# Performance work log

Hardware: AMD Instinct MI355X
Metric: run time of the kernel (lower is better)

Reference implementation:

```python
import jax, jax.numpy as jnp
import numpy as np

D_MODEL, D_K, D_V, H, M = 1024, 64, 64, 16, 40


def setup_inputs() -> dict:
    key = jax.random.key(0)
    ks = jax.random.split(key, 16)
    b, nq, nk = 8, 1024, 1024
    inp = {
        "queries": jax.random.normal(ks[0], (b, nq, D_MODEL), jnp.float32),
        "keys": jax.random.normal(ks[1], (b, nk, D_MODEL), jnp.float32),
        "values": jax.random.normal(ks[2], (b, nk, D_MODEL), jnp.float32),
        "attention_mask": jax.random.randint(ks[3], (b, H, nq, nk), 0, 2) > 0,
        # Linear params, parametrized as x @ W + b (W has shape (in, out)).
        "Wq": jax.random.normal(ks[4], (D_MODEL, H * D_K), jnp.float32) * 0.03,
        "bq": jnp.zeros((H * D_K,), jnp.float32),
        "Wk": jax.random.normal(ks[5], (D_MODEL, H * D_K), jnp.float32) * 0.03,
        "bk": jnp.zeros((H * D_K,), jnp.float32),
        "Wv": jax.random.normal(ks[6], (D_MODEL, H * D_V), jnp.float32) * 0.03,
        "bv": jnp.zeros((H * D_V,), jnp.float32),
        "Wo": jax.random.normal(ks[7], (H * D_V, D_MODEL), jnp.float32) * 0.03,
        "bo": jnp.zeros((D_MODEL,), jnp.float32),
        # Memory slots: m_k ~ N(0, 1/d_k), m_v ~ N(0, 1/m), shape (1, m, h*d)
        "m_k": jax.random.normal(ks[8], (1, M, H * D_K), jnp.float32) / D_K,
        "m_v": jax.random.normal(ks[9], (1, M, H * D_V), jnp.float32) / M,
    }
    return inp


def reference(queries, keys, values, attention_mask, Wq, bq, Wk, bk, Wv, bv, Wo, bo, m_k, m_v):
    b, nq, _ = queries.shape
    nk = keys.shape[1]
    scale = jnp.asarray(np.sqrt(D_K), jnp.float32)

    # scaled memory slots, broadcast over batch
    mk = scale * jnp.broadcast_to(m_k, (b, M, H * D_K))
    mv = jnp.asarray(np.sqrt(M), jnp.float32) * jnp.broadcast_to(m_v, (b, M, H * D_V))

    q = (queries @ Wq + bq).reshape(b, nq, H, D_K).transpose(0, 2, 1, 3)       # b h nq dk
    k = jnp.concatenate([keys @ Wk + bk, mk], axis=1)                           # b (nk+m) h*dk
    k = k.reshape(b, nk + M, H, D_K).transpose(0, 2, 1, 3)                      # b h (nk+m) dk
    v = jnp.concatenate([values @ Wv + bv, mv], axis=1)
    v = v.reshape(b, nk + M, H, D_V).transpose(0, 2, 1, 3)                      # b h (nk+m) dv

    att = jnp.einsum('bhqd,bhkd->bhqk', q, k) / scale                           # b h nq (nk+m)
    # mask only real keys; memory slots always attendable
    att_real = jnp.where(attention_mask, -jnp.inf, att[:, :, :, :nk])
    att = jnp.concatenate([att_real, att[:, :, :, nk:]], axis=-1)
    att = jax.nn.softmax(att, axis=-1)

    out = jnp.einsum('bhqk,bhkd->bhqd', att, v)
    out = out.transpose(0, 2, 1, 3).reshape(b, nq, H * D_V)
    out = out @ Wo + bo
    return out, att
```

## Files before the change

### kernel.cpp

```cpp
#include <hip/hip_runtime.h>
#include <hip/hip_bf16.h>


#define B_ 8
#define NQ 1024
#define NK 1024
#define DM 1024
#define H_ 16
#define DK 64
#define NKM 1064
#define NKP 1104
#define PSTR 280

typedef __attribute__((ext_vector_type(8))) short bf16x8;
typedef __attribute__((ext_vector_type(4))) float f32x4;
typedef __attribute__((ext_vector_type(4))) short short4v;

static __device__ __forceinline__ short f2bf(float x) {
    __hip_bfloat16 h = __float2bfloat16(x);
    return __builtin_bit_cast(short, h);
}
static __device__ __forceinline__ float bf2f(short s) {
    unsigned int u = ((unsigned int)(unsigned short)s) << 16;
    return __builtin_bit_cast(float, u);
}

static __device__ __forceinline__ bf16x8 pack8(const float* __restrict__ p) {
    float4 f0 = *(const float4*)p;
    float4 f1 = *(const float4*)(p + 4);
    bf16x8 a;
    a[0] = f2bf(f0.x); a[1] = f2bf(f0.y); a[2] = f2bf(f0.z); a[3] = f2bf(f0.w);
    a[4] = f2bf(f1.x); a[5] = f2bf(f1.y); a[6] = f2bf(f1.z); a[7] = f2bf(f1.w);
    return a;
}

static __device__ __forceinline__ void gload16(const short* g, short* l) {
    __builtin_amdgcn_global_load_lds(
        (__attribute__((address_space(1))) void*)const_cast<short*>(g),
        (__attribute__((address_space(3))) void*)l, 16, 0, 0);
}

__global__ void detect_mask_kernel(const unsigned int* __restrict__ m, int n_dwords,
                                   int* __restrict__ flag) {
    __shared__ int any_big;
    if (threadIdx.x == 0) any_big = 0;
    __syncthreads();
    for (int i = threadIdx.x; i < n_dwords; i += blockDim.x)
        if (m[i] > 1u) any_big = 1;
    __syncthreads();
    if (threadIdx.x == 0) *flag = any_big ? 0 : 1;
}

__global__ void transpose_w_kernel(const float* __restrict__ W, short* __restrict__ WT) {
    __shared__ float t[32][33];
    int tx = threadIdx.x & 31, ty = threadIdx.x >> 5;
    int k0 = blockIdx.x * 32, n0 = blockIdx.y * 32;
#pragma unroll
    for (int r = 0; r < 4; r++)
        t[ty + 8 * r][tx] = W[(size_t)(k0 + ty + 8 * r) * DM + n0 + tx];
    __syncthreads();
#pragma unroll
    for (int r = 0; r < 4; r++)
        WT[(size_t)(n0 + ty + 8 * r) * DM + k0 + tx] = f2bf(t[tx][ty + 8 * r]);
}

__global__ void convert_bf16_kernel(const float* __restrict__ a, const float* __restrict__ b,
                                    const float* __restrict__ c, short* __restrict__ out) {
    const size_t NT = (size_t)B_ * NQ * DM;
    const size_t total = NT * 3;
    size_t i = ((size_t)blockIdx.x * 256 + threadIdx.x) * 8;
    const size_t step = (size_t)gridDim.x * 256 * 8;
    for (; i < total; i += step) {
        const float* src = (i < NT) ? (a + i) : (i < 2 * NT) ? (b + (i - NT)) : (c + (i - 2 * NT));
        *(bf16x8*)(out + i) = pack8(src);
    }
}

__global__ void fill_mem_kernel(const float* __restrict__ m_k, const float* __restrict__ m_v,
                                short* __restrict__ Kh, short* __restrict__ Vt) {
    int blk = blockIdx.x;
    int bh = blk / 20, rb = blk % 20;
    int r = rb * 4 + (threadIdx.x >> 6);
    int d = threadIdx.x & 63;
    int h = bh & 15;
    float kv = 0.f, vv = 0.f;
    if (r < 40) {
        kv = 8.0f * m_k[(size_t)(r * H_ + h) * DK + d];
        vv = 6.324555320336759f * m_v[(size_t)(r * H_ + h) * DK + d];
    }
    int kk = 1024 + r;
    Kh[((size_t)bh * NKP + kk) * 64 + d] = f2bf(kv);
    Vt[((size_t)bh * 64 + d) * NKP + kk] = f2bf(vv);
}

template <int MODE>
__global__ __launch_bounds__(256) void gemm_tile_kernel(
    const short* __restrict__ Ab, const short* __restrict__ BT,
    const float* __restrict__ bias,
    float* __restrict__ outF, short* __restrict__ outB) {
    __shared__ short As[2][4096];
    __shared__ short Bs[2][4096];

    const int tid = threadIdx.x;
    const int lane = tid & 63;
    const int wid = tid >> 6;
    int swz = (blockIdx.x & 7) * 64 + (blockIdx.x >> 3);
    const int mt = swz >> 3, nt = swz & 7;
    const int brow = mt * 128, bcol = nt * 128;
    const int wr = wid >> 1, wc = wid & 1;
    const int l15 = lane & 15, lg = lane >> 4;

    f32x4 acc[4][4];
#pragma unroll
    for (int m = 0; m < 4; m++)
#pragma unroll
        for (int n = 0; n < 4; n++) acc[m][n] = f32x4{0.f, 0.f, 0.f, 0.f};

    auto stage = [&](int buf, int k0) {
#pragma unroll
        for (int i = 0; i < 2; i++) {
            int c = tid + i * 256;
            int row = c >> 2, slot = c & 3;
            int base = (c & ~63) * 8;
            gload16(Ab + (size_t)(brow + row) * DM + k0 + slot * 8, &As[buf][base]);
            gload16(BT + (size_t)(bcol + row) * DM + k0 + slot * 8, &Bs[buf][base]);
        }
    };

    stage(0, 0);
    for (int kt = 0; kt < 32; ++kt) {
        __syncthreads();
        if (kt + 1 < 32) stage((kt + 1) & 1, (kt + 1) * 32);
        const short* Ab_ = As[kt & 1];
        const short* Bb_ = Bs[kt & 1];
        bf16x8 a[4], b[4];
#pragma unroll
        for (int m = 0; m < 4; m++)
            a[m] = *(const bf16x8*)(Ab_ + (wr * 64 + m * 16 + l15) * 32 + lg * 8);
#pragma unroll
        for (int n = 0; n < 4; n++)
            b[n] = *(const bf16x8*)(Bb_ + (wc * 64 + n * 16 + l15) * 32 + lg * 8);
#pragma unroll
        for (int m = 0; m < 4; m++)
#pragma unroll
            for (int n = 0; n < 4; n++)
                acc[m][n] = __builtin_amdgcn_mfma_f32_16x16x32_bf16(a[m], b[n], acc[m][n], 0, 0, 0);
    }

#pragma unroll
    for (int n = 0; n < 4; n++) {
        int col = bcol + wc * 64 + n * 16 + l15;
        float bval = bias[col];
#pragma unroll
        for (int m = 0; m < 4; m++) {
            int row0 = brow + wr * 64 + m * 16 + lg * 4;
            if (MODE == 3) {
#pragma unroll
                for (int r = 0; r < 4; r++)
                    outF[(size_t)(row0 + r) * DM + col] = acc[m][n][r] + bval;
            } else if (MODE == 0) {
                int h = col >> 6, d = col & 63;
#pragma unroll
                for (int r = 0; r < 4; r++) {
                    int row = row0 + r;
                    int b = row >> 10, q = row & 1023;
                    outB[((size_t)(b * H_ + h) * NQ + q) * 64 + d] = f2bf(acc[m][n][r] + bval);
                }
            } else if (MODE == 1) {
                int h = col >> 6, d = col & 63;
#pragma unroll
                for (int r = 0; r < 4; r++) {
                    int row = row0 + r;
                    int b = row >> 10, kk = row & 1023;
                    outB[((size_t)(b * H_ + h) * NKP + kk) * 64 + d] = f2bf(acc[m][n][r] + bval);
                }
            } else {
                int h = col >> 6, d = col & 63;
                int b = row0 >> 10, kk0 = row0 & 1023;
                short4v sv;
#pragma unroll
                for (int r = 0; r < 4; r++) sv[r] = f2bf(acc[m][n][r] + bval);
                *(short4v*)(outB + ((size_t)(b * H_ + h) * 64 + d) * NKP + kk0) = sv;
            }
        }
    }
}

__global__ __launch_bounds__(256, 4) void attn_fused_kernel(
    const short* __restrict__ Qh, const short* __restrict__ Kh,
    const short* __restrict__ Vt,
    const unsigned char* __restrict__ mb, const int* __restrict__ mi,
    const int* __restrict__ flag,
    float* __restrict__ att, short* __restrict__ Ow) {
    __shared__ short Pl[4][16][PSTR];
    __shared__ float redS[4][16];

    int swz = (blockIdx.x & 7) * 1024 + (blockIdx.x >> 3);
    int bh = swz >> 6;
    int q0 = (swz & 63) * 16;
    int wid = threadIdx.x >> 6;
    int lane = threadIdx.x & 63;
    int l15 = lane & 15, lg = lane >> 4;

    const short* Qb = Qh + (size_t)bh * NQ * 64;
    const short* Kb = Kh + (size_t)bh * NKP * 64;
    const short* Vb = Vt + (size_t)bh * 64 * NKP;
    const int is32 = *flag;

    bf16x8 aq0 = *(const bf16x8*)(Qb + (size_t)(q0 + l15) * 64 + lg * 8);
    bf16x8 aq1 = *(const bf16x8*)(Qb + (size_t)(q0 + l15) * 64 + 32 + lg * 8);

    size_t qrow = (size_t)bh * NQ + q0 + l15;
    const int kkw = wid * 272;
    const int rofs = ((l15 >> 2) << 3) + (l15 & 3);

    f32x4 po[4];
#pragma unroll
    for (int dt = 0; dt < 4; dt++) po[dt] = f32x4{0.f, 0.f, 0.f, 0.f};
    float rs = 0.f;

#pragma unroll 2
    for (int pp = 0; pp < 9; ++pp) {
        int ofs = pp * 32 + lg * 8;
        int base = kkw + pp * 32;
        int kkb = base + lg * 8;
        const short* Kr0 = Kb + (size_t)(base + rofs) * 64;
        bf16x8 k0a = *(const bf16x8*)(Kr0 + lg * 8);
        bf16x8 k0b = *(const bf16x8*)(Kr0 + 32 + lg * 8);
        bf16x8 k1a = *(const bf16x8*)(Kr0 + 256 + lg * 8);
        bf16x8 k1b = *(const bf16x8*)(Kr0 + 256 + 32 + lg * 8);
        bf16x8 bv0 = *(const bf16x8*)(Vb + (size_t)(l15) * NKP + kkb);
        bf16x8 bv1 = *(const bf16x8*)(Vb + (size_t)(16 + l15) * NKP + kkb);
        bf16x8 bv2 = *(const bf16x8*)(Vb + (size_t)(32 + l15) * NKP + kkb);
        bf16x8 bv3 = *(const bf16x8*)(Vb + (size_t)(48 + l15) * NKP + kkb);
        unsigned mlo = 0, mhi = 0;
        if (kkb < NK) {
            if (is32) {
                int4 ma = *(const int4*)(mi + qrow * NK + kkb);
                int4 mc = *(const int4*)(mi + qrow * NK + kkb + 4);
                mlo = (ma.x ? 1u : 0u) | (ma.y ? 0x100u : 0u) |
                      (ma.z ? 0x10000u : 0u) | (ma.w ? 0x1000000u : 0u);
                mhi = (mc.x ? 1u : 0u) | (mc.y ? 0x100u : 0u) |
                      (mc.z ? 0x10000u : 0u) | (mc.w ? 0x1000000u : 0u);
            } else {
                uint2 mu = *(const uint2*)(mb + qrow * NK + kkb);
                mlo = mu.x; mhi = mu.y;
            }
        }
        f32x4 s0 = {0.f, 0.f, 0.f, 0.f}, s1 = {0.f, 0.f, 0.f, 0.f};
        s0 = __builtin_amdgcn_mfma_f32_16x16x32_bf16(k0a, aq0, s0, 0, 0, 0);
        s0 = __builtin_amdgcn_mfma_f32_16x16x32_bf16(k0b, aq1, s0, 0, 0, 0);
        s1 = __builtin_amdgcn_mfma_f32_16x16x32_bf16(k1a, aq0, s1, 0, 0, 0);
        s1 = __builtin_amdgcn_mfma_f32_16x16x32_bf16(k1b, aq1, s1, 0, 0, 0);
        bool live = (kkb < NKM) && (ofs < 272);
        bf16x8 pa;
        float e;
#pragma unroll
        for (int r = 0; r < 4; r++) {
            e = (live && (((mlo >> (8 * r)) & 0xffu) == 0u)) ? __expf(s0[r] * 0.125f) : 0.f;
            rs += e;
            pa[r] = f2bf(e);
        }
#pragma unroll
        for (int r = 0; r < 4; r++) {
            e = (live && (((mhi >> (8 * r)) & 0xffu) == 0u)) ? __expf(s1[r] * 0.125f) : 0.f;
            rs += e;
            pa[4 + r] = f2bf(e);
        }
        po[0] = __builtin_amdgcn_mfma_f32_16x16x32_bf16(pa, bv0, po[0], 0, 0, 0);
        po[1] = __builtin_amdgcn_mfma_f32_16x16x32_bf16(pa, bv1, po[1], 0, 0, 0);
        po[2] = __builtin_amdgcn_mfma_f32_16x16x32_bf16(pa, bv2, po[2], 0, 0, 0);
        po[3] = __builtin_amdgcn_mfma_f32_16x16x32_bf16(pa, bv3, po[3], 0, 0, 0);
        if (ofs < 272)
            *(bf16x8*)(&Pl[wid][l15][ofs]) = pa;
    }

    rs += __shfl_xor(rs, 16);
    rs += __shfl_xor(rs, 32);
    if (lg == 0) redS[wid][l15] = rs;
    __syncthreads();
    float invq = 1.f / (redS[0][l15] + redS[1][l15] + redS[2][l15] + redS[3][l15]);

#pragma unroll 3
    for (int pp = 0; pp < 9; ++pp) {
        int ofs = pp * 32 + lg * 8;
        int kkb = kkw + ofs;
        if (ofs < 272 && kkb < NKM) {
            bf16x8 pa = *(const bf16x8*)(&Pl[wid][l15][ofs]);
            float4 w0, w1;
            w0.x = bf2f(pa[0]) * invq; w0.y = bf2f(pa[1]) * invq;
            w0.z = bf2f(pa[2]) * invq; w0.w = bf2f(pa[3]) * invq;
            w1.x = bf2f(pa[4]) * invq; w1.y = bf2f(pa[5]) * invq;
            w1.z = bf2f(pa[6]) * invq; w1.w = bf2f(pa[7]) * invq;
            *(float4*)(att + qrow * NKM + kkb) = w0;
            *(float4*)(att + qrow * NKM + kkb + 4) = w1;
        }
    }

    float* OredW = (float*)&Pl[wid][0][0];
#pragma unroll
    for (int dt = 0; dt < 4; dt++)
#pragma unroll
        for (int r = 0; r < 4; r++)
            OredW[(lg * 4 + r) * 68 + dt * 16 + l15] = po[dt][r];
    __syncthreads();

    int tq = threadIdx.x >> 4;
    int d0 = (threadIdx.x & 15) * 4;
    float4 o = {0.f, 0.f, 0.f, 0.f};
#pragma unroll
    for (int w = 0; w < 4; w++) {
        const float* Or = (const float*)&Pl[w][0][0];
        float4 v = *(const float4*)(&Or[tq * 68 + d0]);
        o.x += v.x; o.y += v.y; o.z += v.z; o.w += v.w;
    }
    float invt = 1.f / (redS[0][tq] + redS[1][tq] + redS[2][tq] + redS[3][tq]);
    int b = bh >> 4, h = bh & 15;
    short4v sv;
    sv[0] = f2bf(o.x * invt); sv[1] = f2bf(o.y * invt);
    sv[2] = f2bf(o.z * invt); sv[3] = f2bf(o.w * invt);
    *(short4v*)(Ow + ((size_t)b * NQ + q0 + tq) * DM + h * 64 + d0) = sv;
}

extern "C" void kernel_launch(void* const* d_in, const int* in_sizes, int n_in,
                              void* d_out, int out_size, void* d_ws, size_t ws_size,
                              hipStream_t stream) {
    const float* queries = (const float*)d_in[0];
    const float* keys    = (const float*)d_in[1];
    const float* values  = (const float*)d_in[2];
    const void*  mask    = d_in[3];
    const float* Wq = (const float*)d_in[4];
    const float* bq = (const float*)d_in[5];
    const float* Wk = (const float*)d_in[6];
    const float* bk = (const float*)d_in[7];
    const float* Wv = (const float*)d_in[8];
    const float* bv = (const float*)d_in[9];
    const float* Wo = (const float*)d_in[10];
    const float* bo = (const float*)d_in[11];
    const float* m_k = (const float*)d_in[12];
    const float* m_v = (const float*)d_in[13];

    short* WqT = (short*)d_ws;
    short* WkT = WqT + (size_t)DM * DM;
    short* WvT = WkT + (size_t)DM * DM;
    short* WoT = WvT + (size_t)DM * DM;
    short* Qh  = WoT + (size_t)DM * DM;
    short* Kh  = Qh + (size_t)B_ * H_ * NQ * DK;
    short* Vt  = Kh + (size_t)B_ * H_ * NKP * DK;
    short* Ow  = Vt + (size_t)B_ * H_ * DK * NKP;
    char*  after = (char*)(Ow + (size_t)B_ * NQ * DM);
    int*   flag = (int*)after;
    short* Qbf  = (short*)(after + 64);
    short* Kbf  = Qbf + (size_t)B_ * NQ * DM;
    short* Vbf  = Kbf + (size_t)B_ * NQ * DM;

    float* outO = (float*)d_out;
    float* att  = outO + (size_t)B_ * NQ * DM;

    detect_mask_kernel<<<1, 256, 0, stream>>>((const unsigned int*)mask, 4096, flag);

    dim3 tg(32, 32);
    transpose_w_kernel<<<tg, 256, 0, stream>>>(Wq, WqT);
    transpose_w_kernel<<<tg, 256, 0, stream>>>(Wk, WkT);
    transpose_w_kernel<<<tg, 256, 0, stream>>>(Wv, WvT);
    transpose_w_kernel<<<tg, 256, 0, stream>>>(Wo, WoT);

    convert_bf16_kernel<<<4096, 256, 0, stream>>>(queries, keys, values, Qbf);

    gemm_tile_kernel<0><<<512, 256, 0, stream>>>(Qbf, WqT, bq, nullptr, Qh);
    gemm_tile_kernel<1><<<512, 256, 0, stream>>>(Kbf, WkT, bk, nullptr, Kh);
    gemm_tile_kernel<2><<<512, 256, 0, stream>>>(Vbf, WvT, bv, nullptr, Vt);

    fill_mem_kernel<<<2560, 256, 0, stream>>>(m_k, m_v, Kh, Vt);

    attn_fused_kernel<<<8192, 256, 0, stream>>>(Qh, Kh, Vt,
                                                (const unsigned char*)mask, (const int*)mask,
                                                flag, att, Ow);

    gemm_tile_kernel<3><<<512, 256, 0, stream>>>(Ow, WoT, bo, outO, nullptr);
}
```

Measured before the change: 753.1 us.

## Prefetch byte mask up front and store attention tile with block-wide coalesced writes

```diff
diff --git a/kernel.cpp b/kernel.cpp
--- a/kernel.cpp
+++ b/kernel.cpp
@@ -194,6 +194,7 @@
     float* __restrict__ att, short* __restrict__ Ow) {
     __shared__ short Pl[4][16][PSTR];
     __shared__ float redS[4][16];
+    __shared__ float invS[16];
 
     int swz = (blockIdx.x & 7) * 1024 + (blockIdx.x >> 3);
     int bh = swz >> 6;
@@ -213,6 +214,16 @@
     size_t qrow = (size_t)bh * NQ + q0 + l15;
     const int kkw = wid * 272;
     const int rofs = ((l15 >> 2) << 3) + (l15 & 3);
+
+    uint2 mu9[9];
+    if (!is32) {
+#pragma unroll
+        for (int pp = 0; pp < 9; ++pp) {
+            int kkb = kkw + pp * 32 + lg * 8;
+            mu9[pp] = (kkb < NK) ? *(const uint2*)(mb + qrow * NK + kkb)
+                                 : make_uint2(0u, 0u);
+        }
+    }
 
     f32x4 po[4];
 #pragma unroll
@@ -233,19 +244,19 @@
         bf16x8 bv1 = *(const bf16x8*)(Vb + (size_t)(16 + l15) * NKP + kkb);
         bf16x8 bv2 = *(const bf16x8*)(Vb + (size_t)(32 + l15) * NKP + kkb);
         bf16x8 bv3 = *(const bf16x8*)(Vb + (size_t)(48 + l15) * NKP + kkb);
-        unsigned mlo = 0, mhi = 0;
-        if (kkb < NK) {
-            if (is32) {
+        unsigned mlo, mhi;
+        if (is32) {
+            mlo = 0; mhi = 0;
+            if (kkb < NK) {
                 int4 ma = *(const int4*)(mi + qrow * NK + kkb);
                 int4 mc = *(const int4*)(mi + qrow * NK + kkb + 4);
                 mlo = (ma.x ? 1u : 0u) | (ma.y ? 0x100u : 0u) |
                       (ma.z ? 0x10000u : 0u) | (ma.w ? 0x1000000u : 0u);
                 mhi = (mc.x ? 1u : 0u) | (mc.y ? 0x100u : 0u) |
                       (mc.z ? 0x10000u : 0u) | (mc.w ? 0x1000000u : 0u);
-            } else {
-                uint2 mu = *(const uint2*)(mb + qrow * NK + kkb);
-                mlo = mu.x; mhi = mu.y;
             }
+        } else {
+            mlo = mu9[pp].x; mhi = mu9[pp].y;
         }
         f32x4 s0 = {0.f, 0.f, 0.f, 0.f}, s1 = {0.f, 0.f, 0.f, 0.f};
         s0 = __builtin_amdgcn_mfma_f32_16x16x32_bf16(k0a, aq0, s0, 0, 0, 0);
@@ -279,23 +290,28 @@
     rs += __shfl_xor(rs, 32);
     if (lg == 0) redS[wid][l15] = rs;
     __syncthreads();
-    float invq = 1.f / (redS[0][l15] + redS[1][l15] + redS[2][l15] + redS[3][l15]);
-
-#pragma unroll 3
-    for (int pp = 0; pp < 9; ++pp) {
-        int ofs = pp * 32 + lg * 8;
-        int kkb = kkw + ofs;
-        if (ofs < 272 && kkb < NKM) {
-            bf16x8 pa = *(const bf16x8*)(&Pl[wid][l15][ofs]);
-            float4 w0, w1;
-            w0.x = bf2f(pa[0]) * invq; w0.y = bf2f(pa[1]) * invq;
-            w0.z = bf2f(pa[2]) * invq; w0.w = bf2f(pa[3]) * invq;
-            w1.x = bf2f(pa[4]) * invq; w1.y = bf2f(pa[5]) * invq;
-            w1.z = bf2f(pa[6]) * invq; w1.w = bf2f(pa[7]) * invq;
-            *(float4*)(att + qrow * NKM + kkb) = w0;
-            *(float4*)(att + qrow * NKM + kkb + 4) = w1;
-        }
-    }
+    if (threadIdx.x < 16)
+        invS[threadIdx.x] = 1.f / (redS[0][threadIdx.x] + redS[1][threadIdx.x] +
+                                   redS[2][threadIdx.x] + redS[3][threadIdx.x]);
+    __syncthreads();
+
+    float* attT = att + (size_t)(bh * NQ + q0) * NKM;
+#pragma unroll 4
+    for (int j = 0; j < 17; ++j) {
+        int f = j * 256 + threadIdx.x;
+        if (f < 4256) {
+            int r = f / 266;
+            int c = (f - r * 266) * 4;
+            int w = c / 272;
+            int ofs = c - w * 272;
+            short4v p = *(const short4v*)(&Pl[w][r][ofs]);
+            float iv = invS[r];
+            float4 o = {bf2f(p[0]) * iv, bf2f(p[1]) * iv,
+                        bf2f(p[2]) * iv, bf2f(p[3]) * iv};
+            *(float4*)(attT + (size_t)f * 4) = o;
+        }
+    }
+    __syncthreads();
 
     float* OredW = (float*)&Pl[wid][0][0];
 #pragma unroll
@@ -314,7 +330,7 @@
         float4 v = *(const float4*)(&Or[tq * 68 + d0]);
         o.x += v.x; o.y += v.y; o.z += v.z; o.w += v.w;
     }
-    float invt = 1.f / (redS[0][tq] + redS[1][tq] + redS[2][tq] + redS[3][tq]);
+    float invt = invS[tq];
     int b = bh >> 4, h = bh & 15;
     short4v sv;
     sv[0] = f2bf(o.x * invt); sv[1] = f2bf(o.y * invt);
```

After: 716.6 us. -4.9%, faster.
